# Optimization experiments

Measured on AMD Instinct MI355X. Metric: run time of the kernel, lower is better.

The kernel has to match this reference:

```python
import jax, jax.numpy as jnp
import numpy as np

N, IN, OUT, F = 8192, 128, 128, 2
P_EDGE = 0.004  # ~32 neighbors per row


def _sparse_lap(k1, k2):
    mask = jax.random.uniform(k1, (N, N)) < P_EDGE
    mask = mask | jnp.eye(N, dtype=bool)  # nonzero diagonal, like a Laplacian
    vals = jax.random.normal(k2, (N, N), dtype=jnp.float32)
    return jnp.where(mask, vals, 0.0)


def setup_inputs() -> dict:
    key = jax.random.key(0)
    ks = jax.random.split(key, 11)
    x = jax.random.normal(ks[0], (N, IN), dtype=jnp.float32)
    lap_up = _sparse_lap(ks[1], ks[2])
    lap_down = _sparse_lap(ks[3], ks[4])
    proj = jax.random.normal(ks[5], (N, N), dtype=jnp.float32) * np.float32(1.0 / np.sqrt(N))
    scale = np.float32(1.0 / np.sqrt(IN))
    W_up = jax.random.normal(ks[6], (F, IN, OUT), dtype=jnp.float32) * scale
    W_down = jax.random.normal(ks[7], (F, IN, OUT), dtype=jnp.float32) * scale
    a_up = jax.random.normal(ks[8], (2 * OUT * F,), dtype=jnp.float32) * np.float32(0.1)
    a_down = jax.random.normal(ks[9], (2 * OUT * F,), dtype=jnp.float32) * np.float32(0.1)
    W_har = jax.random.normal(ks[10], (IN, OUT), dtype=jnp.float32) * scale
    return dict(x=x, laplacian_up=lap_up, laplacian_down=lap_down, projection_mat=proj,
                W_up=W_up, a_up=a_up, W_down=W_down, a_down=a_down, W_har=W_har)


def _san_conv(x, neighborhood, W, a):
    # W: [F, in, out]; a: [2*out*F]
    n = x.shape[0]
    f, _, out = W.shape
    z = jnp.einsum('ni,fio->fno', x, W)                      # [F, N, out] (x @ weight)
    z_r = jnp.transpose(z, (1, 0, 2)).reshape(n, f * out)    # permute(1,0,2).reshape
    a_src, a_tgt = a[: f * out], a[f * out:]                 # cat([source_j, target_i]) @ a
    s = z_r @ a_src                                          # [N] per-source term
    t = z_r @ a_tgt                                          # [N] per-target term
    mask = neighborhood != 0                                 # sparse pattern of laplacian
    logits = jnp.where(mask, jax.nn.elu(t[:, None] + s[None, :]), -jnp.inf)
    att = jnp.where(mask, jax.nn.softmax(logits, axis=1), 0.0)  # sparse softmax over dim=1
    # sum_{p=1}^{F} att^p @ z[p-1]
    out_msg = jnp.zeros((n, out), dtype=x.dtype)
    A = att
    for p in range(f):
        out_msg = out_msg + A @ z[p]
        if p + 1 < f:
            A = A @ att
    return out_msg


def reference(x, laplacian_up, laplacian_down, projection_mat, W_up, a_up, W_down, a_down, W_har):
    z_down = _san_conv(x, laplacian_down, W_down, a_down)
    z_up = _san_conv(x, laplacian_up, W_up, a_up)
    z_har = projection_mat @ (x @ W_har)
    return z_down + z_up + z_har
```

## Files before the change

### kernel.cpp

```cpp
#include <hip/hip_runtime.h>

#define NN 8192
#define CAP 128
#define PLDA 68
#define PLDB 72

typedef __attribute__((ext_vector_type(8))) short bf16x8;
typedef __attribute__((ext_vector_type(4))) float f32x4;

__device__ __forceinline__ short f2bf(float f) {
    unsigned u = __builtin_bit_cast(unsigned, f);
    u += 0x7FFFu + ((u >> 16) & 1u);
    return (short)(u >> 16);
}

__global__ __launch_bounds__(256) void k_small_gemm(
        const float* __restrict__ x, const float* __restrict__ Wdown,
        const float* __restrict__ Wup, const float* __restrict__ Whar,
        float* __restrict__ zbuf) {
    int wsel = blockIdx.y;
    const float* W = (wsel == 0) ? Wdown : (wsel == 1) ? Wdown + 16384 :
                     (wsel == 2) ? Wup   : (wsel == 3) ? Wup + 16384 : Whar;
    float* out = zbuf + (size_t)wsel * NN * 128;
    __shared__ float Wl[128 * 128];
    __shared__ float Xl[32 * 128];
    int tid = threadIdx.x;
    int row0 = blockIdx.x * 32;
    const float4* W4 = (const float4*)W;
    float4* Wl4 = (float4*)Wl;
    for (int i = tid; i < 4096; i += 256) Wl4[i] = W4[i];
    const float4* X4 = (const float4*)(x + (size_t)row0 * 128);
    float4* Xl4 = (float4*)Xl;
    for (int i = tid; i < 1024; i += 256) Xl4[i] = X4[i];
    __syncthreads();
    int tx = tid & 31, ty = tid >> 5;
    float acc[4][4] = {};
#pragma unroll 2
    for (int i = 0; i < 128; ++i) {
        float w0 = Wl[i * 128 + tx];
        float w1 = Wl[i * 128 + tx + 32];
        float w2 = Wl[i * 128 + tx + 64];
        float w3 = Wl[i * 128 + tx + 96];
#pragma unroll
        for (int rr = 0; rr < 4; ++rr) {
            float xv = Xl[(ty * 4 + rr) * 128 + i];
            acc[rr][0] += xv * w0; acc[rr][1] += xv * w1;
            acc[rr][2] += xv * w2; acc[rr][3] += xv * w3;
        }
    }
#pragma unroll
    for (int rr = 0; rr < 4; ++rr) {
        float* o = out + (size_t)(row0 + ty * 4 + rr) * 128 + tx;
        o[0] = acc[rr][0]; o[32] = acc[rr][1]; o[64] = acc[rr][2]; o[96] = acc[rr][3];
    }
}

__global__ __launch_bounds__(256) void k_st(
        const float* __restrict__ zbuf, const float* __restrict__ a_down,
        const float* __restrict__ a_up, float* __restrict__ stbuf) {
    int sel = blockIdx.y;
    const float* z0 = zbuf + (size_t)sel * 2 * NN * 128;
    const float* z1 = z0 + (size_t)NN * 128;
    const float* a = sel ? a_up : a_down;
    int row = ((int)blockIdx.x * 256 + (int)threadIdx.x) >> 6;
    int lane = threadIdx.x & 63;
    float z0a = z0[(size_t)row * 128 + lane], z0b = z0[(size_t)row * 128 + lane + 64];
    float z1a = z1[(size_t)row * 128 + lane], z1b = z1[(size_t)row * 128 + lane + 64];
    float ps = z0a * a[lane]       + z0b * a[lane + 64]
             + z1a * a[128 + lane] + z1b * a[192 + lane];
    float pt = z0a * a[256 + lane] + z0b * a[320 + lane]
             + z1a * a[384 + lane] + z1b * a[448 + lane];
    for (int off = 32; off; off >>= 1) {
        ps += __shfl_xor(ps, off);
        pt += __shfl_xor(pt, off);
    }
    if (lane == 0) {
        stbuf[(size_t)sel * 2 * NN + row] = ps;
        stbuf[(size_t)sel * 2 * NN + NN + row] = pt;
    }
}

__global__ __launch_bounds__(256) void k_scanatt(
        const float* __restrict__ lapdown, const float* __restrict__ lapup,
        const float* __restrict__ stbuf,
        int* __restrict__ cntbuf, int* __restrict__ colbuf,
        float* __restrict__ valbuf) {
    __shared__ int colsh[4][CAP];
    int sel = blockIdx.y;
    const float* lap = sel ? lapup : lapdown;
    int wid = threadIdx.x >> 6;
    int row = (int)blockIdx.x * 4 + wid;
    int lane = threadIdx.x & 63;
    const float4* lr = (const float4*)(lap + (size_t)row * NN);
    int* crow = colbuf + (size_t)sel * NN * CAP + (size_t)row * CAP;
    int* csh = colsh[wid];
    unsigned long long ltmask = (1ull << lane) - 1ull;
    int c = 0;
    for (int it = 0; it < 32; ++it) {
        float4 v = lr[it * 64 + lane];
#pragma unroll
        for (int q = 0; q < 4; ++q) {
            float f = (q == 0) ? v.x : (q == 1) ? v.y : (q == 2) ? v.z : v.w;
            bool nz = (f != 0.0f);
            unsigned long long m = __ballot(nz);
            if (nz) {
                int slot = c + __popcll(m & ltmask);
                if (slot < CAP) {
                    int cidx = it * 256 + lane * 4 + q;
                    crow[slot] = cidx;
                    csh[slot] = cidx;
                }
            }
            c += __popcll(m);
        }
    }
    int cc = (c < CAP) ? c : CAP;
    int cpad = (cc + 7) & ~7;
    if (lane < cpad - cc) crow[cc + lane] = 0;
    if (lane == 0) cntbuf[sel * NN + row] = cc;
    const float* s = stbuf + (size_t)sel * 2 * NN;
    const float* t = s + NN;
    float* vr = valbuf + (size_t)sel * NN * CAP + (size_t)row * CAP;
    float tv = t[row];
    float e0 = -1e30f, e1 = -1e30f;
    if (lane < cc)      { float v = tv + s[csh[lane]];      e0 = v > 0.f ? v : expm1f(v); }
    if (lane + 64 < cc) { float v = tv + s[csh[lane + 64]]; e1 = v > 0.f ? v : expm1f(v); }
    float m = fmaxf(e0, e1);
    for (int off = 32; off; off >>= 1) m = fmaxf(m, __shfl_xor(m, off));
    float p0 = (lane < cc)      ? expf(e0 - m) : 0.f;
    float p1 = (lane + 64 < cc) ? expf(e1 - m) : 0.f;
    float sum = p0 + p1;
    for (int off = 32; off; off >>= 1) sum += __shfl_xor(sum, off);
    float inv = 1.0f / sum;
    if (lane < cc)      vr[lane] = p0 * inv;
    if (lane + 64 < cc) vr[lane + 64] = p1 * inv;
    if (lane < cpad - cc) vr[cc + lane] = 0.f;
}

__global__ __launch_bounds__(512) void k_tr(
        const float* __restrict__ h, unsigned short* __restrict__ hT) {
    __shared__ unsigned short tile[32 * 128];
    int tid = threadIdx.x;
    int k0 = blockIdx.x * 32;
    int r = tid >> 4;
    int c0 = (tid & 15) * 8;
    const float4* src = (const float4*)(h + (size_t)(k0 + r) * 128 + c0);
    float4 a = src[0], b = src[1];
    unsigned short* tp = &tile[r * 128 + c0];
    tp[0] = (unsigned short)f2bf(a.x); tp[1] = (unsigned short)f2bf(a.y);
    tp[2] = (unsigned short)f2bf(a.z); tp[3] = (unsigned short)f2bf(a.w);
    tp[4] = (unsigned short)f2bf(b.x); tp[5] = (unsigned short)f2bf(b.y);
    tp[6] = (unsigned short)f2bf(b.z); tp[7] = (unsigned short)f2bf(b.w);
    __syncthreads();
    int c = tid & 127;
    int seg = tid >> 7;
    unsigned short v[8];
#pragma unroll
    for (int i = 0; i < 8; ++i) v[i] = tile[(seg * 8 + i) * 128 + c];
    uint4 pack;
    pack.x = (unsigned)v[0] | ((unsigned)v[1] << 16);
    pack.y = (unsigned)v[2] | ((unsigned)v[3] << 16);
    pack.z = (unsigned)v[4] | ((unsigned)v[5] << 16);
    pack.w = (unsigned)v[6] | ((unsigned)v[7] << 16);
    *(uint4*)(hT + (size_t)c * NN + k0 + seg * 8) = pack;
}

__global__ __launch_bounds__(256) void k_proj(
        const float* __restrict__ P, const unsigned short* __restrict__ hT,
        float* __restrict__ partial) {
    __shared__ float As[2][64 * PLDA];
    __shared__ unsigned short Bs[2][128 * PLDB];
    int tid = threadIdx.x;
    int strip = (int)blockIdx.x >> 2;
    int ks = (int)blockIdx.x & 3;
    int RB = strip * 64;
    int k0 = ks * 2048;
    int w = tid >> 6, lane = tid & 63;
    int l15 = lane & 15, koff = (lane >> 4) * 8;
    int ar = tid >> 2, ak = (tid & 3) * 16;
    int bn = tid >> 1, bk = (tid & 1) * 32;
    const float* Ag = P + (size_t)(RB + ar) * NN + k0 + ak;
    const unsigned short* Bg = hT + (size_t)bn * NN + k0 + bk;
    float* Aw0 = &As[0][ar * PLDA + ak];
    unsigned short* Bw0 = &Bs[0][bn * PLDB + bk];
    float* Aw1 = &As[1][ar * PLDA + ak];
    unsigned short* Bw1 = &Bs[1][bn * PLDB + bk];

    float4 sa[4]; uint4 sb[4];
#pragma unroll
    for (int i = 0; i < 4; ++i) sa[i] = *(const float4*)(Ag + i * 4);
#pragma unroll
    for (int i = 0; i < 4; ++i) sb[i] = *(const uint4*)(Bg + i * 8);
#pragma unroll
    for (int i = 0; i < 4; ++i) *(float4*)(Aw0 + i * 4) = sa[i];
#pragma unroll
    for (int i = 0; i < 4; ++i) *(uint4*)(Bw0 + i * 8) = sb[i];
    __syncthreads();

    f32x4 acc[8];
#pragma unroll
    for (int i = 0; i < 8; ++i) acc[i] = (f32x4){0.f, 0.f, 0.f, 0.f};

    for (int t = 0; t < 32; ++t) {
        int cur = t & 1;
        if (t + 1 < 32) {
            const float* Agn = Ag + (t + 1) * 64;
            const unsigned short* Bgn = Bg + (t + 1) * 64;
#pragma unroll
            for (int i = 0; i < 4; ++i) sa[i] = *(const float4*)(Agn + i * 4);
#pragma unroll
            for (int i = 0; i < 4; ++i) sb[i] = *(const uint4*)(Bgn + i * 8);
        }
#pragma unroll
        for (int kk = 0; kk < 2; ++kk) {
            const float* Ab = &As[cur][(w * 16 + l15) * PLDA + kk * 32 + koff];
            float4 a0 = *(const float4*)Ab;
            float4 a1 = *(const float4*)(Ab + 4);
            bf16x8 af;
            af[0] = f2bf(a0.x); af[1] = f2bf(a0.y); af[2] = f2bf(a0.z); af[3] = f2bf(a0.w);
            af[4] = f2bf(a1.x); af[5] = f2bf(a1.y); af[6] = f2bf(a1.z); af[7] = f2bf(a1.w);
#pragma unroll
            for (int ct = 0; ct < 8; ++ct) {
                bf16x8 bf = *(const bf16x8*)(&Bs[cur][(ct * 16 + l15) * PLDB + kk * 32 + koff]);
                acc[ct] = __builtin_amdgcn_mfma_f32_16x16x32_bf16(af, bf, acc[ct], 0, 0, 0);
            }
        }
        if (t + 1 < 32) {
            float* Aw = (cur ? Aw0 : Aw1);
            unsigned short* Bw = (cur ? Bw0 : Bw1);
#pragma unroll
            for (int i = 0; i < 4; ++i) *(float4*)(Aw + i * 4) = sa[i];
#pragma unroll
            for (int i = 0; i < 4; ++i) *(uint4*)(Bw + i * 8) = sb[i];
        }
        __syncthreads();
    }
    float* out = partial + (size_t)ks * NN * 128;
    int prow = RB + w * 16 + (lane >> 4) * 4;
#pragma unroll
    for (int ct = 0; ct < 8; ++ct)
#pragma unroll
        for (int r = 0; r < 4; ++r)
            out[(size_t)(prow + r) * 128 + ct * 16 + l15] = acc[ct][r];
}

__device__ __forceinline__ void edge_acc(
        int c, const int* __restrict__ cr, const float* __restrict__ vr,
        const float* __restrict__ B, int lane, float& ax, float& ay) {
    int cpad = (c + 7) & ~7;
    for (int e = 0; e < cpad; e += 8) {
        int4   j0 = *(const int4*)(cr + e);
        int4   j1 = *(const int4*)(cr + e + 4);
        float4 v0 = *(const float4*)(vr + e);
        float4 v1 = *(const float4*)(vr + e + 4);
        float2 b0 = ((const float2*)(B + (size_t)j0.x * 128))[lane];
        float2 b1 = ((const float2*)(B + (size_t)j0.y * 128))[lane];
        float2 b2 = ((const float2*)(B + (size_t)j0.z * 128))[lane];
        float2 b3 = ((const float2*)(B + (size_t)j0.w * 128))[lane];
        float2 b4 = ((const float2*)(B + (size_t)j1.x * 128))[lane];
        float2 b5 = ((const float2*)(B + (size_t)j1.y * 128))[lane];
        float2 b6 = ((const float2*)(B + (size_t)j1.z * 128))[lane];
        float2 b7 = ((const float2*)(B + (size_t)j1.w * 128))[lane];
        ax += v0.x * b0.x; ay += v0.x * b0.y;
        ax += v0.y * b1.x; ay += v0.y * b1.y;
        ax += v0.z * b2.x; ay += v0.z * b2.y;
        ax += v0.w * b3.x; ay += v0.w * b3.y;
        ax += v1.x * b4.x; ay += v1.x * b4.y;
        ax += v1.y * b5.x; ay += v1.y * b5.y;
        ax += v1.z * b6.x; ay += v1.z * b6.y;
        ax += v1.w * b7.x; ay += v1.w * b7.y;
    }
}

__global__ __launch_bounds__(256) void k_pass1(
        const int* __restrict__ cnt, const int* __restrict__ col,
        const float* __restrict__ val, const float* __restrict__ zbuf,
        float* __restrict__ wbuf) {
    int sel = blockIdx.y;
    const float* z0 = zbuf + (size_t)sel * 2 * NN * 128;
    const float* z1 = z0 + (size_t)NN * 128;
    float* w = wbuf + (size_t)sel * NN * 128;
    int row = ((int)blockIdx.x * 256 + (int)threadIdx.x) >> 6;
    int lane = threadIdx.x & 63;
    int c = cnt[sel * NN + row];
    float2 a = ((const float2*)(z0 + (size_t)row * 128))[lane];
    float ax = a.x, ay = a.y;
    edge_acc(c, col + ((size_t)sel * NN + row) * CAP,
             val + ((size_t)sel * NN + row) * CAP, z1, lane, ax, ay);
    ((float2*)(w + (size_t)row * 128))[lane] = make_float2(ax, ay);
}

__global__ __launch_bounds__(256) void k_final(
        const int* __restrict__ cnt, const int* __restrict__ col,
        const float* __restrict__ val, const float* __restrict__ wbuf,
        const float* __restrict__ partial, float* __restrict__ out) {
    int row = ((int)blockIdx.x * 256 + (int)threadIdx.x) >> 6;
    int lane = threadIdx.x & 63;
    float ax = 0.f, ay = 0.f;
#pragma unroll
    for (int ks = 0; ks < 4; ++ks) {
        float2 p = ((const float2*)(partial + (size_t)ks * NN * 128 + (size_t)row * 128))[lane];
        ax += p.x; ay += p.y;
    }
    edge_acc(cnt[row], col + (size_t)row * CAP, val + (size_t)row * CAP,
             wbuf, lane, ax, ay);
    edge_acc(cnt[NN + row], col + ((size_t)NN + row) * CAP,
             val + ((size_t)NN + row) * CAP, wbuf + (size_t)NN * 128, lane, ax, ay);
    ((float2*)(out + (size_t)row * 128))[lane] = make_float2(ax, ay);
}

extern "C" void kernel_launch(void* const* d_in, const int* in_sizes, int n_in,
                              void* d_out, int out_size, void* d_ws, size_t ws_size,
                              hipStream_t stream) {
    const float* x        = (const float*)d_in[0];
    const float* lap_up   = (const float*)d_in[1];
    const float* lap_down = (const float*)d_in[2];
    const float* proj     = (const float*)d_in[3];
    const float* W_up     = (const float*)d_in[4];
    const float* a_up     = (const float*)d_in[5];
    const float* W_down   = (const float*)d_in[6];
    const float* a_down   = (const float*)d_in[7];
    const float* W_har    = (const float*)d_in[8];
    float* out = (float*)d_out;
    float* ws = (float*)d_ws;

    const size_t ZSZ = (size_t)NN * 128;
    size_t off = 0;
    float* zbuf = ws + off;              off += 5 * ZSZ;
    float* stbuf = ws + off;             off += 4 * NN;
    int* cntbuf = (int*)(ws + off);      off += 2 * NN;
    int* colbuf = (int*)(ws + off);      off += 2 * ZSZ;
    float* valbuf = ws + off;            off += 2 * ZSZ;
    float* wbuf = ws + off;              off += 2 * ZSZ;
    unsigned short* hT = (unsigned short*)(ws + off); off += ZSZ / 2;
    float* partial = ws + off;           off += 4 * ZSZ;

    hipLaunchKernelGGL(k_small_gemm, dim3(256, 5), dim3(256), 0, stream,
                       x, W_down, W_up, W_har, zbuf);
    hipLaunchKernelGGL(k_st, dim3(2048, 2), dim3(256), 0, stream,
                       zbuf, a_down, a_up, stbuf);
    hipLaunchKernelGGL(k_scanatt, dim3(2048, 2), dim3(256), 0, stream,
                       lap_down, lap_up, stbuf, cntbuf, colbuf, valbuf);
    hipLaunchKernelGGL(k_tr, dim3(256), dim3(512), 0, stream,
                       zbuf + 4 * ZSZ, hT);
    hipLaunchKernelGGL(k_proj, dim3(512), dim3(256), 0, stream,
                       proj, hT, partial);
    hipLaunchKernelGGL(k_pass1, dim3(2048, 2), dim3(256), 0, stream,
                       cntbuf, colbuf, valbuf, zbuf, wbuf);
    hipLaunchKernelGGL(k_final, dim3(2048), dim3(256), 0, stream,
                       cntbuf, colbuf, valbuf, wbuf, partial, out);
}
```

Measured before the change: 820.9 us.

## Fuse attention score dot products into small GEMM and widen sparse gathers

The per-row source/target attention terms are now computed in the epilogue of the small GEMM from register accumulators, as per-filter partial sums that the scan kernel adds. This removes the separate k_st kernel and its re-read of the z buffers. The sparse gather helper now takes 16 edges per step into two independent accumulator pairs, with padding raised to 16. pass1 handles the down and up operators in one launch with interleaved gathers. The changes aim to cut a launch and memory traffic and add memory-level parallelism, at the cost of more registers and extra zero-padded edges.

Result: no change. 824.5 us (+0.4%).

```diff
diff --git a/kernel.cpp b/kernel.cpp
--- a/kernel.cpp
+++ b/kernel.cpp
@@ -17,7 +17,8 @@
 __global__ __launch_bounds__(256) void k_small_gemm(
         const float* __restrict__ x, const float* __restrict__ Wdown,
         const float* __restrict__ Wup, const float* __restrict__ Whar,
-        float* __restrict__ zbuf) {
+        const float* __restrict__ a_down, const float* __restrict__ a_up,
+        float* __restrict__ zbuf, float* __restrict__ stP) {
     int wsel = blockIdx.y;
     const float* W = (wsel == 0) ? Wdown : (wsel == 1) ? Wdown + 16384 :
                      (wsel == 2) ? Wup   : (wsel == 3) ? Wup + 16384 : Whar;
@@ -53,36 +54,37 @@
         float* o = out + (size_t)(row0 + ty * 4 + rr) * 128 + tx;
         o[0] = acc[rr][0]; o[32] = acc[rr][1]; o[64] = acc[rr][2]; o[96] = acc[rr][3];
     }
-}
-
-__global__ __launch_bounds__(256) void k_st(
-        const float* __restrict__ zbuf, const float* __restrict__ a_down,
-        const float* __restrict__ a_up, float* __restrict__ stbuf) {
-    int sel = blockIdx.y;
-    const float* z0 = zbuf + (size_t)sel * 2 * NN * 128;
-    const float* z1 = z0 + (size_t)NN * 128;
-    const float* a = sel ? a_up : a_down;
-    int row = ((int)blockIdx.x * 256 + (int)threadIdx.x) >> 6;
-    int lane = threadIdx.x & 63;
-    float z0a = z0[(size_t)row * 128 + lane], z0b = z0[(size_t)row * 128 + lane + 64];
-    float z1a = z1[(size_t)row * 128 + lane], z1b = z1[(size_t)row * 128 + lane + 64];
-    float ps = z0a * a[lane]       + z0b * a[lane + 64]
-             + z1a * a[128 + lane] + z1b * a[192 + lane];
-    float pt = z0a * a[256 + lane] + z0b * a[320 + lane]
-             + z1a * a[384 + lane] + z1b * a[448 + lane];
-    for (int off = 32; off; off >>= 1) {
-        ps += __shfl_xor(ps, off);
-        pt += __shfl_xor(pt, off);
-    }
-    if (lane == 0) {
-        stbuf[(size_t)sel * 2 * NN + row] = ps;
-        stbuf[(size_t)sel * 2 * NN + NN + row] = pt;
+    if (wsel < 4) {
+        const float* a = (wsel < 2) ? a_down : a_up;
+        int f = wsel & 1;
+        float asv[4], atv[4];
+#pragma unroll
+        for (int q = 0; q < 4; ++q) {
+            asv[q] = a[f * 128 + tx + q * 32];
+            atv[q] = a[256 + f * 128 + tx + q * 32];
+        }
+#pragma unroll
+        for (int rr = 0; rr < 4; ++rr) {
+            float ps = acc[rr][0] * asv[0] + acc[rr][1] * asv[1]
+                     + acc[rr][2] * asv[2] + acc[rr][3] * asv[3];
+            float pt = acc[rr][0] * atv[0] + acc[rr][1] * atv[1]
+                     + acc[rr][2] * atv[2] + acc[rr][3] * atv[3];
+            for (int w = 16; w; w >>= 1) {
+                ps += __shfl_xor(ps, w);
+                pt += __shfl_xor(pt, w);
+            }
+            if (tx == 0) {
+                int row = row0 + ty * 4 + rr;
+                stP[(size_t)wsel * NN + row] = ps;
+                stP[(size_t)(4 + wsel) * NN + row] = pt;
+            }
+        }
     }
 }
 
 __global__ __launch_bounds__(256) void k_scanatt(
         const float* __restrict__ lapdown, const float* __restrict__ lapup,
-        const float* __restrict__ stbuf,
+        const float* __restrict__ stP,
         int* __restrict__ cntbuf, int* __restrict__ colbuf,
         float* __restrict__ valbuf) {
     __shared__ int colsh[4][CAP];
@@ -115,16 +117,27 @@
         }
     }
     int cc = (c < CAP) ? c : CAP;
-    int cpad = (cc + 7) & ~7;
+    int cpad = (cc + 15) & ~15;
+    if (cpad > CAP) cpad = CAP;
     if (lane < cpad - cc) crow[cc + lane] = 0;
     if (lane == 0) cntbuf[sel * NN + row] = cc;
-    const float* s = stbuf + (size_t)sel * 2 * NN;
-    const float* t = s + NN;
+    const float* sP0 = stP + (size_t)(2 * sel) * NN;
+    const float* sP1 = sP0 + NN;
+    const float* tP0 = stP + (size_t)(4 + 2 * sel) * NN;
+    const float* tP1 = tP0 + NN;
     float* vr = valbuf + (size_t)sel * NN * CAP + (size_t)row * CAP;
-    float tv = t[row];
+    float tv = tP0[row] + tP1[row];
     float e0 = -1e30f, e1 = -1e30f;
-    if (lane < cc)      { float v = tv + s[csh[lane]];      e0 = v > 0.f ? v : expm1f(v); }
-    if (lane + 64 < cc) { float v = tv + s[csh[lane + 64]]; e1 = v > 0.f ? v : expm1f(v); }
+    if (lane < cc) {
+        int j = csh[lane];
+        float v = tv + sP0[j] + sP1[j];
+        e0 = v > 0.f ? v : expm1f(v);
+    }
+    if (lane + 64 < cc) {
+        int j = csh[lane + 64];
+        float v = tv + sP0[j] + sP1[j];
+        e1 = v > 0.f ? v : expm1f(v);
+    }
     float m = fmaxf(e0, e1);
     for (int off = 32; off; off >>= 1) m = fmaxf(m, __shfl_xor(m, off));
     float p0 = (lane < cc)      ? expf(e0 - m) : 0.f;
@@ -244,31 +257,32 @@
             out[(size_t)(prow + r) * 128 + ct * 16 + l15] = acc[ct][r];
 }
 
-__device__ __forceinline__ void edge_acc(
-        int c, const int* __restrict__ cr, const float* __restrict__ vr,
-        const float* __restrict__ B, int lane, float& ax, float& ay) {
-    int cpad = (c + 7) & ~7;
-    for (int e = 0; e < cpad; e += 8) {
-        int4   j0 = *(const int4*)(cr + e);
-        int4   j1 = *(const int4*)(cr + e + 4);
-        float4 v0 = *(const float4*)(vr + e);
-        float4 v1 = *(const float4*)(vr + e + 4);
-        float2 b0 = ((const float2*)(B + (size_t)j0.x * 128))[lane];
-        float2 b1 = ((const float2*)(B + (size_t)j0.y * 128))[lane];
-        float2 b2 = ((const float2*)(B + (size_t)j0.z * 128))[lane];
-        float2 b3 = ((const float2*)(B + (size_t)j0.w * 128))[lane];
-        float2 b4 = ((const float2*)(B + (size_t)j1.x * 128))[lane];
-        float2 b5 = ((const float2*)(B + (size_t)j1.y * 128))[lane];
-        float2 b6 = ((const float2*)(B + (size_t)j1.z * 128))[lane];
-        float2 b7 = ((const float2*)(B + (size_t)j1.w * 128))[lane];
-        ax += v0.x * b0.x; ay += v0.x * b0.y;
-        ax += v0.y * b1.x; ay += v0.y * b1.y;
-        ax += v0.z * b2.x; ay += v0.z * b2.y;
-        ax += v0.w * b3.x; ay += v0.w * b3.y;
-        ax += v1.x * b4.x; ay += v1.x * b4.y;
-        ax += v1.y * b5.x; ay += v1.y * b5.y;
-        ax += v1.z * b6.x; ay += v1.z * b6.y;
-        ax += v1.w * b7.x; ay += v1.w * b7.y;
+__device__ __forceinline__ void gather16(
+        const int* __restrict__ cr, const float* __restrict__ vr,
+        const float* __restrict__ B, int lane,
+        float& ax0, float& ay0, float& ax1, float& ay1) {
+#pragma unroll
+    for (int h = 0; h < 2; ++h) {
+        int4   ja = *(const int4*)(cr + h * 8);
+        int4   jb = *(const int4*)(cr + h * 8 + 4);
+        float4 va = *(const float4*)(vr + h * 8);
+        float4 vb = *(const float4*)(vr + h * 8 + 4);
+        float2 b0 = ((const float2*)(B + (size_t)ja.x * 128))[lane];
+        float2 b1 = ((const float2*)(B + (size_t)ja.y * 128))[lane];
+        float2 b2 = ((const float2*)(B + (size_t)ja.z * 128))[lane];
+        float2 b3 = ((const float2*)(B + (size_t)ja.w * 128))[lane];
+        float2 b4 = ((const float2*)(B + (size_t)jb.x * 128))[lane];
+        float2 b5 = ((const float2*)(B + (size_t)jb.y * 128))[lane];
+        float2 b6 = ((const float2*)(B + (size_t)jb.z * 128))[lane];
+        float2 b7 = ((const float2*)(B + (size_t)jb.w * 128))[lane];
+        ax0 += va.x * b0.x; ay0 += va.x * b0.y;
+        ax1 += va.y * b1.x; ay1 += va.y * b1.y;
+        ax0 += va.z * b2.x; ay0 += va.z * b2.y;
+        ax1 += va.w * b3.x; ay1 += va.w * b3.y;
+        ax0 += vb.x * b4.x; ay0 += vb.x * b4.y;
+        ax1 += vb.y * b5.x; ay1 += vb.y * b5.y;
+        ax0 += vb.z * b6.x; ay0 += vb.z * b6.y;
+        ax1 += vb.w * b7.x; ay1 += vb.w * b7.y;
     }
 }
 
@@ -276,18 +290,28 @@
         const int* __restrict__ cnt, const int* __restrict__ col,
         const float* __restrict__ val, const float* __restrict__ zbuf,
         float* __restrict__ wbuf) {
-    int sel = blockIdx.y;
-    const float* z0 = zbuf + (size_t)sel * 2 * NN * 128;
-    const float* z1 = z0 + (size_t)NN * 128;
-    float* w = wbuf + (size_t)sel * NN * 128;
     int row = ((int)blockIdx.x * 256 + (int)threadIdx.x) >> 6;
     int lane = threadIdx.x & 63;
-    int c = cnt[sel * NN + row];
-    float2 a = ((const float2*)(z0 + (size_t)row * 128))[lane];
-    float ax = a.x, ay = a.y;
-    edge_acc(c, col + ((size_t)sel * NN + row) * CAP,
-             val + ((size_t)sel * NN + row) * CAP, z1, lane, ax, ay);
-    ((float2*)(w + (size_t)row * 128))[lane] = make_float2(ax, ay);
+    const size_t ZS = (size_t)NN * 128;
+    int cD = cnt[row], cU = cnt[NN + row];
+    int padD = (cD + 15) & ~15, padU = (cU + 15) & ~15;
+    const int*   crD = col + (size_t)row * CAP;
+    const int*   crU = col + ((size_t)NN + row) * CAP;
+    const float* vrD = val + (size_t)row * CAP;
+    const float* vrU = val + ((size_t)NN + row) * CAP;
+    float2 iD = ((const float2*)(zbuf + (size_t)row * 128))[lane];
+    float2 iU = ((const float2*)(zbuf + 2 * ZS + (size_t)row * 128))[lane];
+    float axD0 = iD.x, ayD0 = iD.y, axD1 = 0.f, ayD1 = 0.f;
+    float axU0 = iU.x, ayU0 = iU.y, axU1 = 0.f, ayU1 = 0.f;
+    int emax = padD > padU ? padD : padU;
+    for (int e = 0; e < emax; e += 16) {
+        if (e < padD)
+            gather16(crD + e, vrD + e, zbuf + ZS, lane, axD0, ayD0, axD1, ayD1);
+        if (e < padU)
+            gather16(crU + e, vrU + e, zbuf + 3 * ZS, lane, axU0, ayU0, axU1, ayU1);
+    }
+    ((float2*)(wbuf + (size_t)row * 128))[lane] = make_float2(axD0 + axD1, ayD0 + ayD1);
+    ((float2*)(wbuf + ZS + (size_t)row * 128))[lane] = make_float2(axU0 + axU1, ayU0 + ayU1);
 }
 
 __global__ __launch_bounds__(256) void k_final(
@@ -296,17 +320,28 @@
         const float* __restrict__ partial, float* __restrict__ out) {
     int row = ((int)blockIdx.x * 256 + (int)threadIdx.x) >> 6;
     int lane = threadIdx.x & 63;
-    float ax = 0.f, ay = 0.f;
-#pragma unroll
-    for (int ks = 0; ks < 4; ++ks) {
-        float2 p = ((const float2*)(partial + (size_t)ks * NN * 128 + (size_t)row * 128))[lane];
-        ax += p.x; ay += p.y;
-    }
-    edge_acc(cnt[row], col + (size_t)row * CAP, val + (size_t)row * CAP,
-             wbuf, lane, ax, ay);
-    edge_acc(cnt[NN + row], col + ((size_t)NN + row) * CAP,
-             val + ((size_t)NN + row) * CAP, wbuf + (size_t)NN * 128, lane, ax, ay);
-    ((float2*)(out + (size_t)row * 128))[lane] = make_float2(ax, ay);
+    const size_t ZS = (size_t)NN * 128;
+    float ax0 = 0.f, ay0 = 0.f, ax1 = 0.f, ay1 = 0.f;
+#pragma unroll
+    for (int ks = 0; ks < 4; ks += 2) {
+        float2 p0 = ((const float2*)(partial + (size_t)ks * ZS + (size_t)row * 128))[lane];
+        float2 p1 = ((const float2*)(partial + (size_t)(ks + 1) * ZS + (size_t)row * 128))[lane];
+        ax0 += p0.x; ay0 += p0.y; ax1 += p1.x; ay1 += p1.y;
+    }
+    int cD = cnt[row], cU = cnt[NN + row];
+    int padD = (cD + 15) & ~15, padU = (cU + 15) & ~15;
+    const int*   crD = col + (size_t)row * CAP;
+    const int*   crU = col + ((size_t)NN + row) * CAP;
+    const float* vrD = val + (size_t)row * CAP;
+    const float* vrU = val + ((size_t)NN + row) * CAP;
+    int emax = padD > padU ? padD : padU;
+    for (int e = 0; e < emax; e += 16) {
+        if (e < padD)
+            gather16(crD + e, vrD + e, wbuf, lane, ax0, ay0, ax1, ay1);
+        if (e < padU)
+            gather16(crU + e, vrU + e, wbuf + ZS, lane, ax0, ay0, ax1, ay1);
+    }
+    ((float2*)(out + (size_t)row * 128))[lane] = make_float2(ax0 + ax1, ay0 + ay1);
 }
 
 extern "C" void kernel_launch(void* const* d_in, const int* in_sizes, int n_in,
@@ -327,7 +362,7 @@
     const size_t ZSZ = (size_t)NN * 128;
     size_t off = 0;
     float* zbuf = ws + off;              off += 5 * ZSZ;
-    float* stbuf = ws + off;             off += 4 * NN;
+    float* stbuf = ws + off;             off += 8 * NN;
     int* cntbuf = (int*)(ws + off);      off += 2 * NN;
     int* colbuf = (int*)(ws + off);      off += 2 * ZSZ;
     float* valbuf = ws + off;            off += 2 * ZSZ;
@@ -336,16 +371,14 @@
     float* partial = ws + off;           off += 4 * ZSZ;
 
     hipLaunchKernelGGL(k_small_gemm, dim3(256, 5), dim3(256), 0, stream,
-                       x, W_down, W_up, W_har, zbuf);
-    hipLaunchKernelGGL(k_st, dim3(2048, 2), dim3(256), 0, stream,
-                       zbuf, a_down, a_up, stbuf);
+                       x, W_down, W_up, W_har, a_down, a_up, zbuf, stbuf);
     hipLaunchKernelGGL(k_scanatt, dim3(2048, 2), dim3(256), 0, stream,
                        lap_down, lap_up, stbuf, cntbuf, colbuf, valbuf);
     hipLaunchKernelGGL(k_tr, dim3(256), dim3(512), 0, stream,
                        zbuf + 4 * ZSZ, hT);
     hipLaunchKernelGGL(k_proj, dim3(512), dim3(256), 0, stream,
                        proj, hT, partial);
-    hipLaunchKernelGGL(k_pass1, dim3(2048, 2), dim3(256), 0, stream,
+    hipLaunchKernelGGL(k_pass1, dim3(2048), dim3(256), 0, stream,
                        cntbuf, colbuf, valbuf, zbuf, wbuf);
     hipLaunchKernelGGL(k_final, dim3(2048), dim3(256), 0, stream,
                        cntbuf, colbuf, valbuf, wbuf, partial, out);
```
